# Optimization experiments

Measured on AMD Instinct MI355X. Metric: run time of the kernel, lower is better.

Reference implementation:

```python
import jax, jax.numpy as jnp
import numpy as np

ALPHA = 0.001
RHO = 0.05


def setup_inputs() -> dict:
    key = jax.random.key(0)
    ks = jax.random.split(key, 7)
    S, B, H, L = 1024, 64, 512, 2
    sc = 1.0 / np.sqrt(H)  # torch Linear default init scale
    inputs = jax.random.normal(ks[0], (S, B, H), jnp.float32)
    times = jnp.arange(S, dtype=jnp.float32)
    Wxh_w = jax.random.uniform(ks[1], (L, 4 * H, H), jnp.float32, -sc, sc)
    Wxh_b = jax.random.uniform(ks[2], (L, 4 * H), jnp.float32, -sc, sc)
    Whh_w = jax.random.uniform(ks[3], (L, 4 * H, H), jnp.float32, -sc, sc)
    tau = jax.random.normal(ks[4], (L, H), jnp.float32) * 0.5 + 5.0
    s_p = jax.random.uniform(ks[5], (L, H), jnp.float32) * tau
    return dict(inputs=inputs, times=times, Wxh_w=Wxh_w, Wxh_b=Wxh_b,
                Whh_w=Whh_w, tau=tau, s_p=s_p)


def _time_gate(t, s, tau):
    # phi in [0,1): phase of the oscillation; k is the triangular open-gate
    phi = jnp.fmod(t - s, tau) / tau
    k = jnp.where(phi < RHO / 2.0,
                  2.0 * phi / RHO,
                  jnp.where(phi < RHO, 2.0 - 2.0 * phi / RHO, ALPHA * phi))
    return jax.lax.stop_gradient(k)  # computed under torch.no_grad in source


def reference(inputs, times, Wxh_w, Wxh_b, Whh_w, tau, s_p):
    L, H4, _ = Wxh_w.shape
    H = H4 // 4
    S, B, _ = inputs.shape
    h0 = jnp.zeros((L, B, H), inputs.dtype)
    c0 = jnp.zeros((L, B, H), inputs.dtype)

    def step(carry, xt):
        h, c = carry
        x, t = xt  # x: [B, I], t: scalar time
        new_h, new_c = [], []
        inp = x
        for l in range(L):
            gates = inp @ Wxh_w[l].T + Wxh_b[l] + h[l] @ Whh_w[l].T  # [B, 4H]
            i, f, g, o = jnp.split(gates, 4, axis=1)
            k = _time_gate(t, s_p[l], tau[l])  # [H], broadcasts over batch
            ft = jax.nn.sigmoid(f + 1.0 - k)
            it = jax.nn.sigmoid(i) * k
            gt = jnp.tanh(g) * k
            ot = jax.nn.sigmoid(o) * k
            cy = ft * c[l] + it * gt
            hy = ot * jnp.tanh(cy)
            new_h.append(hy)
            new_c.append(cy)
            inp = hy
        h2 = jnp.stack(new_h)
        c2 = jnp.stack(new_c)
        return (h2, c2), h2[-1]

    (h, c), outputs = jax.lax.scan(step, (h0, c0), (inputs, times))
    return outputs, h, c
```

## Files before the change

kernel.cpp:

```cpp
#include <hip/hip_runtime.h>


#define TPREC 8

#define OFF_H0    4096
#define OFF_H1    266240
#define OFF_H0F   528384
#define OFF_H1F   1052672
#define OFF_C0    1576960
#define OFF_C1    1708032
#define OFF_XPRE  1839104
#define OFF_KTAB  2887680
#define OFF_W0    7081984
#define OFF_W1    9179136
#define OFF_WX    13373440

#define HB_SLOT   65536
#define HF_SLOT   131072
#define XP_SLOT   524288

typedef float  f32x4  __attribute__((ext_vector_type(4)));
typedef int    i32x4  __attribute__((ext_vector_type(4)));
typedef __bf16 bf16x8 __attribute__((ext_vector_type(8)));

static __device__ __forceinline__ unsigned short f2bf(float f) {
  unsigned u = __builtin_bit_cast(unsigned, f);
  u += 0x7FFFu + ((u >> 16) & 1u);
  return (unsigned short)(u >> 16);
}
static __device__ __forceinline__ float sigm(float x) { return 1.0f / (1.0f + __expf(-x)); }
static __device__ __forceinline__ float tanhfast(float x) { return 1.0f - 2.0f / (__expf(2.0f * x) + 1.0f); }

static __device__ __forceinline__ i32x4 ring_load16(const void* p) {
  return *(const i32x4*)p;
}
static __device__ __forceinline__ float ring_loadf(const void* p) {
  return *(const float*)p;
}
static __device__ __forceinline__ void ring_storef(void* p, float v) {
  *(float*)p = v;
}
static __device__ __forceinline__ void ring_store_u16(void* p, unsigned v) {
  *(unsigned short*)p = (unsigned short)v;
}

static __device__ __forceinline__ f32x4 mfma16(bf16x8 a, bf16x8 b, f32x4 c) {
  return __builtin_amdgcn_mfma_f32_16x16x32_bf16(a, b, c, 0, 0, 0);
}
static __device__ __forceinline__ bf16x8 lds_frag(const char* p) {
  return __builtin_bit_cast(bf16x8, *(const i32x4*)p);
}

__global__ void plstm_prep(const float* __restrict__ Wxh_w, const float* __restrict__ Whh_w,
                           const float* __restrict__ times, const float* __restrict__ tau,
                           const float* __restrict__ s_p, unsigned char* __restrict__ ws) {
  const int idx = blockIdx.x * 256 + threadIdx.x;
  const int stride = gridDim.x * 256;
  for (int e = idx; e < 1048576; e += stride) {
    int g = e >> 16, j = (e >> 9) & 127, k = e & 511;
    int gate = j >> 5, u = g * 32 + (j & 31);
    ((unsigned short*)(ws + OFF_W0))[e] = f2bf(Whh_w[(gate * 512 + u) * 512 + k]);
  }
  for (int e = idx; e < 2097152; e += stride) {
    int g = e >> 16, j = (e >> 10) & 63, k = e & 1023;
    int gate = j >> 4, row = gate * 512 + g * 16 + (j & 15);
    float v = (k < 512) ? Wxh_w[1048576 + row * 512 + k] : Whh_w[1048576 + row * 512 + (k - 512)];
    ((unsigned short*)(ws + OFF_W1))[e] = f2bf(v);
  }
  for (int e = idx; e < 1048576; e += stride) {
    int g = e >> 16, j = (e >> 9) & 127, k = e & 511;
    ((unsigned short*)(ws + OFF_WX))[e] = f2bf(Wxh_w[(g * 128 + j) * 512 + k]);
  }
  for (int e = idx; e < 1048576; e += stride) {
    int t = e >> 10, r = e & 1023, l = r >> 9, u = r & 511;
    float phi = fmodf(times[t] - s_p[l * 512 + u], tau[l * 512 + u]) / tau[l * 512 + u];
    float kv;
    if (phi < 0.025f)      kv = phi * 40.0f;
    else if (phi < 0.05f)  kv = 2.0f - phi * 40.0f;
    else                   kv = 0.001f * phi;
    ((float*)(ws + OFF_KTAB))[e] = kv;
  }
}

__global__ void __launch_bounds__(256, 1)
plstm_step(const float* __restrict__ xin, const float* __restrict__ bias,
           const float* __restrict__ Wxh_w, const float* __restrict__ Whh_w,
           float* __restrict__ out, unsigned char* __restrict__ wsu, int q) {
  __shared__ char Wl[131072];
  __shared__ char Al[16384];

  const char* ws = (const char*)wsu;
  char* wsw = (char*)wsu;
  const int bid = blockIdx.x, tid = threadIdx.x;
  const int lane = tid & 63, wv = tid >> 6;
  const int lq = lane >> 4, lr = lane & 15;
  const int role = (bid < 16) ? 0 : (bid < 48) ? 1 : 2;
  const int grp = (role == 0) ? bid : (role == 1) ? bid - 16 : bid - 48;

  if (role == 0 && (q < 1 || q > 1024)) return;
  if (role == 1 && (q < 2 || q > 1025)) return;
  if (role == 2 && q > 1023) return;

  const float* ktabp = (const float*)(ws + OFF_KTAB);
  const float* bias0 = bias;
  const float* bias1 = bias + 2048;
  float* Alf = (float*)Al;

  {
    const char* wsrc = ws +
      ((role == 0) ? (OFF_W0 + grp * 131072) : (role == 1) ? (OFF_W1 + grp * 131072)
                                             : (OFF_WX + grp * 131072));
    const int kshift = (role == 1) ? 10 : 9;
    for (int e = tid * 8; e < 65536; e += 2048) {
      i32x4 v = *(const i32x4*)(wsrc + e * 2);
      int row = e >> kshift;
      *(i32x4*)(Wl + ((e * 2) ^ ((row & 7) << 4))) = v;
    }
    __syncthreads();
  }

  if (role == 0) {
    {
      const int t0 = q - 1;
      const char* xpre = ws + OFF_XPRE + (t0 & 1) * XP_SLOT;
      char* c0p = wsw + OFF_C0;
      char* h0bw = wsw + OFF_H0 + (t0 & 1) * HB_SLOT;

      if (t0 <= TPREC) {
        const int rp = tid >> 4, bq = tid & 15;
        const int gate = rp >> 2;
        const int u0 = grp * 32 + (rp & 3) * 8;
        const float* w8 = Whh_w + (size_t)(gate * 512 + u0) * 512;
        const char* hsrc = ws + OFF_H0F + ((t0 - 1) & 1) * HF_SLOT;
        f32x4 acc8[8] = {};
        for (int kc = 0; kc < 8; ++kc) {
          __syncthreads();
          for (int i = 0; i < 4; ++i) {
            int qi = tid + 256 * i, k = qi >> 4, b4 = qi & 15;
            i32x4 v = ring_load16(hsrc + ((kc * 64 + k) * 64 + b4 * 4) * 4);
            *(i32x4*)(Alf + k * 64 + b4 * 4) = v;
          }
          __syncthreads();
          for (int kb = 0; kb < 16; ++kb) {
            f32x4 w4[8];
#pragma unroll
            for (int r = 0; r < 8; ++r) w4[r] = *(const f32x4*)(w8 + r * 512 + kc * 64 + kb * 4);
#pragma unroll
            for (int ks = 0; ks < 4; ++ks) {
              f32x4 hv = *(const f32x4*)(Alf + (kb * 4 + ks) * 64 + bq * 4);
#pragma unroll
              for (int r = 0; r < 8; ++r) acc8[r] += w4[r][ks] * hv;
            }
          }
        }
        char* h0fw = wsw + OFF_H0F + (t0 & 1) * HF_SLOT;
        for (int ph = 0; ph < 2; ++ph) {
          __syncthreads();
          if ((bq >> 3) == ph) {
#pragma unroll
            for (int r = 0; r < 8; ++r)
              *(f32x4*)(Alf + (rp * 8 + r) * 32 + (bq & 7) * 4) = acc8[r];
          }
          __syncthreads();
          for (int i = 0; i < 4; ++i) {
            int e = tid + 256 * i;
            int u = e >> 5, b32 = e & 31, b = ph * 32 + b32;
            int ucol = grp * 32 + u;
            float g4[4];
#pragma unroll
            for (int gt = 0; gt < 4; ++gt)
              g4[gt] = Alf[(gt * 32 + u) * 32 + b32]
                     + ring_loadf(xpre + (b * 2048 + gt * 512 + ucol) * 4);
            const float kk = ktabp[t0 * 1024 + ucol];
            const float cold = *(const float*)(c0p + (b * 512 + ucol) * 4);
            const float itg = sigm(g4[0]) * kk;
            const float ftg = sigm(g4[1] + 1.0f - kk);
            const float gtg = tanhfast(g4[2]) * kk;
            const float otg = sigm(g4[3]) * kk;
            const float cn = ftg * cold + itg * gtg;
            const float hn = otg * tanhfast(cn);
            *(float*)(c0p + (b * 512 + ucol) * 4) = cn;
            ring_store_u16(h0bw + (b * 512 + ucol) * 2, (unsigned)f2bf(hn));
            ring_storef(h0fw + (ucol * 64 + b) * 4, hn);
          }
        }
      } else {
        const int uf = wv >> 1, mh = wv & 1;
        const int ucol = grp * 32 + uf * 16 + lr;
        float xp[2][4][4];
#pragma unroll
        for (int m = 0; m < 2; ++m)
#pragma unroll
          for (int i = 0; i < 4; ++i) {
            const int b = mh * 32 + m * 16 + lq * 4 + i;
#pragma unroll
            for (int gt = 0; gt < 4; ++gt)
              xp[m][gt][i] = ring_loadf(xpre + (b * 2048 + gt * 512 + ucol) * 4);
          }
        const char* ahi = ws + OFF_H0 + ((t0 - 1) & 1) * HB_SLOT;
        i32x4 areg[16];
#pragma unroll
        for (int kc = 0; kc < 4; ++kc)
#pragma unroll
          for (int it = 0; it < 4; ++it) {
            const int idx = it * 2048 + tid * 8, row = idx >> 7, col = idx & 127;
            areg[kc * 4 + it] = ring_load16(ahi + (row * 512 + kc * 128 + col) * 2);
          }
        const float kk = ktabp[t0 * 1024 + ucol];
        float cold[2][4];
#pragma unroll
        for (int m = 0; m < 2; ++m)
#pragma unroll
          for (int i = 0; i < 4; ++i) {
            const int b = mh * 32 + m * 16 + lq * 4 + i;
            cold[m][i] = *(const float*)(c0p + (b * 512 + ucol) * 4);
          }
        char* c0pw = wsw + OFF_C0;
        f32x4 acc[2][4] = {};
#pragma unroll
        for (int kc = 0; kc < 4; ++kc) {
          __syncthreads();
#pragma unroll
          for (int it = 0; it < 4; ++it) {
            const int idx = it * 2048 + tid * 8, row = idx >> 7, col = idx & 127;
            *(i32x4*)(Al + (((row * 128 + col) * 2) ^ ((row & 7) << 4))) = areg[kc * 4 + it];
          }
          __syncthreads();
#pragma unroll
          for (int ks = 0; ks < 4; ++ks) {
            bf16x8 af[2];
#pragma unroll
            for (int m = 0; m < 2; ++m) {
              const int b = mh * 32 + m * 16 + lr;
              af[m] = lds_frag(Al + (((b * 128 + ks * 32 + lq * 8) * 2) ^ ((b & 7) << 4)));
            }
#pragma unroll
            for (int gt = 0; gt < 4; ++gt) {
              const int j = gt * 32 + uf * 16 + lr;
              const bf16x8 bf = lds_frag(Wl + (((j * 512 + kc * 128 + ks * 32 + lq * 8) * 2) ^ ((j & 7) << 4)));
              acc[0][gt] = mfma16(af[0], bf, acc[0][gt]);
              acc[1][gt] = mfma16(af[1], bf, acc[1][gt]);
            }
          }
        }
#pragma unroll
        for (int m = 0; m < 2; ++m)
#pragma unroll
          for (int i = 0; i < 4; ++i) {
            const int b = mh * 32 + m * 16 + lq * 4 + i;
            const float gi = acc[m][0][i] + xp[m][0][i];
            const float gf = acc[m][1][i] + xp[m][1][i];
            const float gz = acc[m][2][i] + xp[m][2][i];
            const float go = acc[m][3][i] + xp[m][3][i];
            const float itg = sigm(gi) * kk;
            const float ftg = sigm(gf + 1.0f - kk);
            const float gtg = tanhfast(gz) * kk;
            const float otg = sigm(go) * kk;
            const float cn = ftg * cold[m][i] + itg * gtg;
            const float hn = otg * tanhfast(cn);
            *(float*)(c0pw + (b * 512 + ucol) * 4) = cn;
            ring_store_u16(h0bw + (b * 512 + ucol) * 2, (unsigned)f2bf(hn));
            if (t0 == 1023) {
              out[33554432 + b * 512 + ucol] = hn;
              out[33554432 + 65536 + b * 512 + ucol] = cn;
            }
          }
      }
    }
  } else if (role == 1) {
    {
      const int t1 = q - 2;
      char* c1p = wsw + OFF_C1;
      char* h1bw = wsw + OFF_H1 + (t1 & 1) * HB_SLOT;

      if (t1 <= TPREC) {
        const int rp = tid >> 4, bq = tid & 15;
        const int gate = rp >> 2;
        const int uoff0 = (rp & 3) * 4;
        const float* wx4 = Wxh_w + 1048576 + (size_t)(gate * 512 + grp * 16 + uoff0) * 512;
        const float* wh4 = Whh_w + 1048576 + (size_t)(gate * 512 + grp * 16 + uoff0) * 512;
        const char* s0f = ws + OFF_H0F + (t1 & 1) * HF_SLOT;
        const char* s1f = ws + OFF_H1F + ((t1 - 1) & 1) * HF_SLOT;
        f32x4 acc4[4] = {};
        for (int kc = 0; kc < 16; ++kc) {
          const char* hsrc = (kc < 8) ? s0f : s1f;
          const int k0 = (kc & 7) * 64;
          const float* wsel = (kc < 8) ? (wx4 + k0) : (wh4 + k0);
          __syncthreads();
          for (int i = 0; i < 4; ++i) {
            int qi = tid + 256 * i, k = qi >> 4, b4 = qi & 15;
            i32x4 v = ring_load16(hsrc + ((k0 + k) * 64 + b4 * 4) * 4);
            *(i32x4*)(Alf + k * 64 + b4 * 4) = v;
          }
          __syncthreads();
          for (int kb = 0; kb < 16; ++kb) {
            f32x4 w4[4];
#pragma unroll
            for (int r = 0; r < 4; ++r) w4[r] = *(const f32x4*)(wsel + r * 512 + kb * 4);
#pragma unroll
            for (int ks = 0; ks < 4; ++ks) {
              f32x4 hv = *(const f32x4*)(Alf + (kb * 4 + ks) * 64 + bq * 4);
#pragma unroll
              for (int r = 0; r < 4; ++r) acc4[r] += w4[r][ks] * hv;
            }
          }
        }
        char* h1fw = wsw + OFF_H1F + (t1 & 1) * HF_SLOT;
        __syncthreads();
#pragma unroll
        for (int r = 0; r < 4; ++r)
          *(f32x4*)(Alf + (rp * 4 + r) * 64 + bq * 4) = acc4[r];
        __syncthreads();
        for (int i = 0; i < 4; ++i) {
          int e = tid + 256 * i;
          int u = e >> 6, b = e & 63;
          int ucol = grp * 16 + u;
          float g4[4];
#pragma unroll
          for (int gt = 0; gt < 4; ++gt)
            g4[gt] = Alf[(gt * 16 + u) * 64 + b] + bias1[gt * 512 + ucol];
          const float kk = ktabp[t1 * 1024 + 512 + ucol];
          const float cold = *(const float*)(c1p + (b * 512 + ucol) * 4);
          const float itg = sigm(g4[0]) * kk;
          const float ftg = sigm(g4[1] + 1.0f - kk);
          const float gtg = tanhfast(g4[2]) * kk;
          const float otg = sigm(g4[3]) * kk;
          const float cn = ftg * cold + itg * gtg;
          const float hn = otg * tanhfast(cn);
          *(float*)(c1p + (b * 512 + ucol) * 4) = cn;
          ring_store_u16(h1bw + (b * 512 + ucol) * 2, (unsigned)f2bf(hn));
          ring_storef(h1fw + (ucol * 64 + b) * 4, hn);
          out[t1 * 32768 + b * 512 + ucol] = hn;
        }
      } else {
        const int ucol = grp * 16 + lr;
        float bs[4];
#pragma unroll
        for (int gt = 0; gt < 4; ++gt) bs[gt] = bias1[gt * 512 + ucol];
        const float kk = ktabp[t1 * 1024 + 512 + ucol];
        const char* s0 = ws + OFF_H0 + (t1 & 1) * HB_SLOT;
        const char* s1 = ws + OFF_H1 + ((t1 - 1) & 1) * HB_SLOT;
        i32x4 areg[32];
#pragma unroll
        for (int kc = 0; kc < 8; ++kc) {
          const char* s = (kc < 4) ? s0 : s1;
          const int kb = (kc & 3) * 128;
#pragma unroll
          for (int it = 0; it < 4; ++it) {
            const int idx = it * 2048 + tid * 8, row = idx >> 7, col = idx & 127;
            areg[kc * 4 + it] = ring_load16(s + (row * 512 + kb + col) * 2);
          }
        }
        float cold[4];
#pragma unroll
        for (int i = 0; i < 4; ++i) {
          const int b = wv * 16 + lq * 4 + i;
          cold[i] = *(const float*)(c1p + (b * 512 + ucol) * 4);
        }
        f32x4 acc[4] = {};
#pragma unroll
        for (int kc = 0; kc < 8; ++kc) {
          __syncthreads();
#pragma unroll
          for (int it = 0; it < 4; ++it) {
            const int idx = it * 2048 + tid * 8, row = idx >> 7, col = idx & 127;
            *(i32x4*)(Al + (((row * 128 + col) * 2) ^ ((row & 7) << 4))) = areg[kc * 4 + it];
          }
          __syncthreads();
#pragma unroll
          for (int ks = 0; ks < 4; ++ks) {
            const int b = wv * 16 + lr;
            const bf16x8 af = lds_frag(Al + (((b * 128 + ks * 32 + lq * 8) * 2) ^ ((b & 7) << 4)));
#pragma unroll
            for (int gt = 0; gt < 4; ++gt) {
              const int j = gt * 16 + lr;
              const bf16x8 bf = lds_frag(Wl + (((j * 1024 + kc * 128 + ks * 32 + lq * 8) * 2) ^ ((j & 7) << 4)));
              acc[gt] = mfma16(af, bf, acc[gt]);
            }
          }
        }
#pragma unroll
        for (int i = 0; i < 4; ++i) {
          const int b = wv * 16 + lq * 4 + i;
          const float gi = acc[0][i] + bs[0];
          const float gf = acc[1][i] + bs[1];
          const float gz = acc[2][i] + bs[2];
          const float go = acc[3][i] + bs[3];
          const float itg = sigm(gi) * kk;
          const float ftg = sigm(gf + 1.0f - kk);
          const float gtg = tanhfast(gz) * kk;
          const float otg = sigm(go) * kk;
          const float cn = ftg * cold[i] + itg * gtg;
          const float hn = otg * tanhfast(cn);
          *(float*)(c1p + (b * 512 + ucol) * 4) = cn;
          ring_store_u16(h1bw + (b * 512 + ucol) * 2, (unsigned)f2bf(hn));
          out[t1 * 32768 + b * 512 + ucol] = hn;
          if (t1 == 1023) {
            out[33554432 + 32768 + b * 512 + ucol] = hn;
            out[33554432 + 65536 + 32768 + b * 512 + ucol] = cn;
          }
        }
      }
    }
  } else {
    {
      const float* xs = xin + (size_t)q * 32768;
      char* xw = wsw + OFF_XPRE + (q & 1) * XP_SLOT;

      if (q <= TPREC) {
        const int rp = tid >> 4, bq = tid & 15;
        const int n0 = grp * 128 + rp * 8;
        const float* w8 = Wxh_w + (size_t)n0 * 512;
        f32x4 acc8[8] = {};
        for (int kc = 0; kc < 8; ++kc) {
          __syncthreads();
          for (int i = 0; i < 4; ++i) {
            int qi = tid + 256 * i, b = qi >> 4, k4 = qi & 15;
            f32x4 v = *(const f32x4*)(xs + b * 512 + kc * 64 + k4 * 4);
#pragma unroll
            for (int j = 0; j < 4; ++j) Alf[(k4 * 4 + j) * 64 + b] = v[j];
          }
          __syncthreads();
          for (int kb = 0; kb < 16; ++kb) {
            f32x4 w4[8];
#pragma unroll
            for (int r = 0; r < 8; ++r) w4[r] = *(const f32x4*)(w8 + r * 512 + kc * 64 + kb * 4);
#pragma unroll
            for (int ks = 0; ks < 4; ++ks) {
              f32x4 hv = *(const f32x4*)(Alf + (kb * 4 + ks) * 64 + bq * 4);
#pragma unroll
              for (int r = 0; r < 8; ++r) acc8[r] += w4[r][ks] * hv;
            }
          }
        }
#pragma unroll
        for (int r = 0; r < 8; ++r) {
          const int n = n0 + r;
          const float bv = bias0[n];
#pragma unroll
          for (int j = 0; j < 4; ++j)
            ring_storef(xw + ((bq * 4 + j) * 2048 + n) * 4, acc8[r][j] + bv);
        }
      } else {
        float b0v[2];
#pragma unroll
        for (int nf = 0; nf < 2; ++nf) b0v[nf] = bias0[grp * 128 + wv * 32 + nf * 16 + lr];
        f32x4 xr[4][4][2];
#pragma unroll
        for (int kc = 0; kc < 4; ++kc)
#pragma unroll
          for (int it = 0; it < 4; ++it) {
            const int idx = it * 2048 + tid * 8, row = idx >> 7, col = idx & 127;
            const float* p = xs + row * 512 + kc * 128 + col;
            xr[kc][it][0] = *(const f32x4*)p;
            xr[kc][it][1] = *(const f32x4*)(p + 4);
          }
        f32x4 acc[4][2] = {};
#pragma unroll
        for (int kc = 0; kc < 4; ++kc) {
          __syncthreads();
#pragma unroll
          for (int it = 0; it < 4; ++it) {
            const int idx = it * 2048 + tid * 8, row = idx >> 7, col = idx & 127;
            i32x4 v;
#pragma unroll
            for (int w2 = 0; w2 < 4; ++w2) {
              const float x0 = xr[kc][it][w2 >> 1][(w2 & 1) * 2 + 0];
              const float x1 = xr[kc][it][w2 >> 1][(w2 & 1) * 2 + 1];
              v[w2] = (int)((unsigned)f2bf(x0) | ((unsigned)f2bf(x1) << 16));
            }
            *(i32x4*)(Al + (((row * 128 + col) * 2) ^ ((row & 7) << 4))) = v;
          }
          __syncthreads();
#pragma unroll
          for (int ks = 0; ks < 4; ++ks) {
            bf16x8 af[4];
#pragma unroll
            for (int m = 0; m < 4; ++m) {
              const int b = m * 16 + lr;
              af[m] = lds_frag(Al + (((b * 128 + ks * 32 + lq * 8) * 2) ^ ((b & 7) << 4)));
            }
#pragma unroll
            for (int nf = 0; nf < 2; ++nf) {
              const int j = wv * 32 + nf * 16 + lr;
              const bf16x8 bf = lds_frag(Wl + (((j * 512 + kc * 128 + ks * 32 + lq * 8) * 2) ^ ((j & 7) << 4)));
#pragma unroll
              for (int m = 0; m < 4; ++m) acc[m][nf] = mfma16(af[m], bf, acc[m][nf]);
            }
          }
        }
#pragma unroll
        for (int m = 0; m < 4; ++m)
#pragma unroll
          for (int nf = 0; nf < 2; ++nf)
#pragma unroll
            for (int i = 0; i < 4; ++i) {
              const int b = m * 16 + lq * 4 + i;
              const int n = grp * 128 + wv * 32 + nf * 16 + lr;
              ring_storef(xw + (b * 2048 + n) * 4, acc[m][nf][i] + b0v[nf]);
            }
      }
    }
  }
}

extern "C" void kernel_launch(void* const* d_in, const int* in_sizes, int n_in,
                              void* d_out, int out_size, void* d_ws, size_t ws_size,
                              hipStream_t stream) {
  (void)in_sizes; (void)n_in; (void)out_size; (void)ws_size;
  const float* inputs = (const float*)d_in[0];
  const float* times  = (const float*)d_in[1];
  const float* Wxh_w  = (const float*)d_in[2];
  const float* Wxh_b  = (const float*)d_in[3];
  const float* Whh_w  = (const float*)d_in[4];
  const float* tau    = (const float*)d_in[5];
  const float* s_p    = (const float*)d_in[6];
  unsigned char* ws = (unsigned char*)d_ws;
  float* out = (float*)d_out;

  hipMemsetAsync(ws + OFF_H0 + HB_SLOT, 0, HB_SLOT, stream);
  hipMemsetAsync(ws + OFF_H1 + HB_SLOT, 0, HB_SLOT, stream);
  hipMemsetAsync(ws + OFF_H0F + HF_SLOT, 0, HF_SLOT, stream);
  hipMemsetAsync(ws + OFF_H1F + HF_SLOT, 0, HF_SLOT, stream);
  hipMemsetAsync(ws + OFF_C0, 0, 131072, stream);
  hipMemsetAsync(ws + OFF_C1, 0, 131072, stream);

  plstm_prep<<<8192, 256, 0, stream>>>(Wxh_w, Whh_w, times, tau, s_p, ws);

  for (int q = 0; q <= 1025; ++q)
    plstm_step<<<64, 256, 0, stream>>>(inputs, Wxh_b, Wxh_w, Whh_w, out, ws, q);
}
```

Baseline: 12.69 ms.

## Load MFMA operands directly from global memory instead of staging through LDS

Removes the per-launch copy of each block's 128KB weight slice into shared memory and the LDS staging of the hidden/input activation tiles. Each wave now fetches its bf16 A and B fragments straight from global memory (relying on L2/cache), and the input-projection path converts fp32 to bf16 on the fly per fragment. This drops a large LDS fill and several block barriers per step launch, at the cost of redundant, less coalesced global reads across waves.

New measurement: 24.66 ms. 94.3% more time.

```diff
diff --git a/kernel.cpp b/kernel.cpp
--- a/kernel.cpp
+++ b/kernel.cpp
@@ -28,6 +28,9 @@
   u += 0x7FFFu + ((u >> 16) & 1u);
   return (unsigned short)(u >> 16);
 }
+static __device__ __forceinline__ int pack2(float a, float b) {
+  return (int)((unsigned)f2bf(a) | ((unsigned)f2bf(b) << 16));
+}
 static __device__ __forceinline__ float sigm(float x) { return 1.0f / (1.0f + __expf(-x)); }
 static __device__ __forceinline__ float tanhfast(float x) { return 1.0f - 2.0f / (__expf(2.0f * x) + 1.0f); }
 
@@ -47,8 +50,8 @@
 static __device__ __forceinline__ f32x4 mfma16(bf16x8 a, bf16x8 b, f32x4 c) {
   return __builtin_amdgcn_mfma_f32_16x16x32_bf16(a, b, c, 0, 0, 0);
 }
-static __device__ __forceinline__ bf16x8 lds_frag(const char* p) {
-  return __builtin_bit_cast(bf16x8, *(const i32x4*)p);
+static __device__ __forceinline__ bf16x8 asbf(i32x4 v) {
+  return __builtin_bit_cast(bf16x8, v);
 }
 
 __global__ void plstm_prep(const float* __restrict__ Wxh_w, const float* __restrict__ Whh_w,
@@ -86,7 +89,6 @@
 plstm_step(const float* __restrict__ xin, const float* __restrict__ bias,
            const float* __restrict__ Wxh_w, const float* __restrict__ Whh_w,
            float* __restrict__ out, unsigned char* __restrict__ wsu, int q) {
-  __shared__ char Wl[131072];
   __shared__ char Al[16384];
 
   const char* ws = (const char*)wsu;
@@ -105,19 +107,6 @@
   const float* bias0 = bias;
   const float* bias1 = bias + 2048;
   float* Alf = (float*)Al;
-
-  {
-    const char* wsrc = ws +
-      ((role == 0) ? (OFF_W0 + grp * 131072) : (role == 1) ? (OFF_W1 + grp * 131072)
-                                             : (OFF_WX + grp * 131072));
-    const int kshift = (role == 1) ? 10 : 9;
-    for (int e = tid * 8; e < 65536; e += 2048) {
-      i32x4 v = *(const i32x4*)(wsrc + e * 2);
-      int row = e >> kshift;
-      *(i32x4*)(Wl + ((e * 2) ^ ((row & 7) << 4))) = v;
-    }
-    __syncthreads();
-  }
 
   if (role == 0) {
     {
@@ -187,6 +176,7 @@
       } else {
         const int uf = wv >> 1, mh = wv & 1;
         const int ucol = grp * 32 + uf * 16 + lr;
+        const char* w0src = ws + OFF_W0 + grp * 131072;
         float xp[2][4][4];
 #pragma unroll
         for (int m = 0; m < 2; ++m)
@@ -198,14 +188,6 @@
               xp[m][gt][i] = ring_loadf(xpre + (b * 2048 + gt * 512 + ucol) * 4);
           }
         const char* ahi = ws + OFF_H0 + ((t0 - 1) & 1) * HB_SLOT;
-        i32x4 areg[16];
-#pragma unroll
-        for (int kc = 0; kc < 4; ++kc)
-#pragma unroll
-          for (int it = 0; it < 4; ++it) {
-            const int idx = it * 2048 + tid * 8, row = idx >> 7, col = idx & 127;
-            areg[kc * 4 + it] = ring_load16(ahi + (row * 512 + kc * 128 + col) * 2);
-          }
         const float kk = ktabp[t0 * 1024 + ucol];
         float cold[2][4];
 #pragma unroll
@@ -215,29 +197,22 @@
             const int b = mh * 32 + m * 16 + lq * 4 + i;
             cold[m][i] = *(const float*)(c0p + (b * 512 + ucol) * 4);
           }
-        char* c0pw = wsw + OFF_C0;
         f32x4 acc[2][4] = {};
 #pragma unroll
         for (int kc = 0; kc < 4; ++kc) {
-          __syncthreads();
-#pragma unroll
-          for (int it = 0; it < 4; ++it) {
-            const int idx = it * 2048 + tid * 8, row = idx >> 7, col = idx & 127;
-            *(i32x4*)(Al + (((row * 128 + col) * 2) ^ ((row & 7) << 4))) = areg[kc * 4 + it];
-          }
-          __syncthreads();
 #pragma unroll
           for (int ks = 0; ks < 4; ++ks) {
+            const int ko = kc * 128 + ks * 32 + lq * 8;
             bf16x8 af[2];
 #pragma unroll
             for (int m = 0; m < 2; ++m) {
               const int b = mh * 32 + m * 16 + lr;
-              af[m] = lds_frag(Al + (((b * 128 + ks * 32 + lq * 8) * 2) ^ ((b & 7) << 4)));
+              af[m] = asbf(ring_load16(ahi + (b * 512 + ko) * 2));
             }
 #pragma unroll
             for (int gt = 0; gt < 4; ++gt) {
               const int j = gt * 32 + uf * 16 + lr;
-              const bf16x8 bf = lds_frag(Wl + (((j * 512 + kc * 128 + ks * 32 + lq * 8) * 2) ^ ((j & 7) << 4)));
+              const bf16x8 bf = asbf(ring_load16(w0src + (j * 512 + ko) * 2));
               acc[0][gt] = mfma16(af[0], bf, acc[0][gt]);
               acc[1][gt] = mfma16(af[1], bf, acc[1][gt]);
             }
@@ -258,7 +233,7 @@
             const float otg = sigm(go) * kk;
             const float cn = ftg * cold[m][i] + itg * gtg;
             const float hn = otg * tanhfast(cn);
-            *(float*)(c0pw + (b * 512 + ucol) * 4) = cn;
+            *(float*)(c0p + (b * 512 + ucol) * 4) = cn;
             ring_store_u16(h0bw + (b * 512 + ucol) * 2, (unsigned)f2bf(hn));
             if (t0 == 1023) {
               out[33554432 + b * 512 + ucol] = hn;
@@ -334,47 +309,33 @@
         }
       } else {
         const int ucol = grp * 16 + lr;
+        const char* w1src = ws + OFF_W1 + grp * 131072;
         float bs[4];
 #pragma unroll
         for (int gt = 0; gt < 4; ++gt) bs[gt] = bias1[gt * 512 + ucol];
         const float kk = ktabp[t1 * 1024 + 512 + ucol];
         const char* s0 = ws + OFF_H0 + (t1 & 1) * HB_SLOT;
         const char* s1 = ws + OFF_H1 + ((t1 - 1) & 1) * HB_SLOT;
-        i32x4 areg[32];
+        const int brow = wv * 16 + lr;
+        float cold[4];
+#pragma unroll
+        for (int i = 0; i < 4; ++i) {
+          const int b = wv * 16 + lq * 4 + i;
+          cold[i] = *(const float*)(c1p + (b * 512 + ucol) * 4);
+        }
+        f32x4 acc[4] = {};
 #pragma unroll
         for (int kc = 0; kc < 8; ++kc) {
           const char* s = (kc < 4) ? s0 : s1;
           const int kb = (kc & 3) * 128;
 #pragma unroll
-          for (int it = 0; it < 4; ++it) {
-            const int idx = it * 2048 + tid * 8, row = idx >> 7, col = idx & 127;
-            areg[kc * 4 + it] = ring_load16(s + (row * 512 + kb + col) * 2);
-          }
-        }
-        float cold[4];
-#pragma unroll
-        for (int i = 0; i < 4; ++i) {
-          const int b = wv * 16 + lq * 4 + i;
-          cold[i] = *(const float*)(c1p + (b * 512 + ucol) * 4);
-        }
-        f32x4 acc[4] = {};
-#pragma unroll
-        for (int kc = 0; kc < 8; ++kc) {
-          __syncthreads();
-#pragma unroll
-          for (int it = 0; it < 4; ++it) {
-            const int idx = it * 2048 + tid * 8, row = idx >> 7, col = idx & 127;
-            *(i32x4*)(Al + (((row * 128 + col) * 2) ^ ((row & 7) << 4))) = areg[kc * 4 + it];
-          }
-          __syncthreads();
-#pragma unroll
           for (int ks = 0; ks < 4; ++ks) {
-            const int b = wv * 16 + lr;
-            const bf16x8 af = lds_frag(Al + (((b * 128 + ks * 32 + lq * 8) * 2) ^ ((b & 7) << 4)));
+            const int ko = kb + ks * 32 + lq * 8;
+            const bf16x8 af = asbf(ring_load16(s + (brow * 512 + ko) * 2));
 #pragma unroll
             for (int gt = 0; gt < 4; ++gt) {
               const int j = gt * 16 + lr;
-              const bf16x8 bf = lds_frag(Wl + (((j * 1024 + kc * 128 + ks * 32 + lq * 8) * 2) ^ ((j & 7) << 4)));
+              const bf16x8 bf = asbf(ring_load16(w1src + (j * 1024 + kc * 128 + ks * 32 + lq * 8) * 2));
               acc[gt] = mfma16(af, bf, acc[gt]);
             }
           }
@@ -442,48 +403,31 @@
             ring_storef(xw + ((bq * 4 + j) * 2048 + n) * 4, acc8[r][j] + bv);
         }
       } else {
+        const char* wxsrc = ws + OFF_WX + grp * 131072;
         float b0v[2];
 #pragma unroll
         for (int nf = 0; nf < 2; ++nf) b0v[nf] = bias0[grp * 128 + wv * 32 + nf * 16 + lr];
-        f32x4 xr[4][4][2];
-#pragma unroll
-        for (int kc = 0; kc < 4; ++kc)
-#pragma unroll
-          for (int it = 0; it < 4; ++it) {
-            const int idx = it * 2048 + tid * 8, row = idx >> 7, col = idx & 127;
-            const float* p = xs + row * 512 + kc * 128 + col;
-            xr[kc][it][0] = *(const f32x4*)p;
-            xr[kc][it][1] = *(const f32x4*)(p + 4);
-          }
         f32x4 acc[4][2] = {};
 #pragma unroll
         for (int kc = 0; kc < 4; ++kc) {
-          __syncthreads();
-#pragma unroll
-          for (int it = 0; it < 4; ++it) {
-            const int idx = it * 2048 + tid * 8, row = idx >> 7, col = idx & 127;
-            i32x4 v;
-#pragma unroll
-            for (int w2 = 0; w2 < 4; ++w2) {
-              const float x0 = xr[kc][it][w2 >> 1][(w2 & 1) * 2 + 0];
-              const float x1 = xr[kc][it][w2 >> 1][(w2 & 1) * 2 + 1];
-              v[w2] = (int)((unsigned)f2bf(x0) | ((unsigned)f2bf(x1) << 16));
-            }
-            *(i32x4*)(Al + (((row * 128 + col) * 2) ^ ((row & 7) << 4))) = v;
-          }
-          __syncthreads();
 #pragma unroll
           for (int ks = 0; ks < 4; ++ks) {
+            const int ko = kc * 128 + ks * 32 + lq * 8;
             bf16x8 af[4];
 #pragma unroll
             for (int m = 0; m < 4; ++m) {
-              const int b = m * 16 + lr;
-              af[m] = lds_frag(Al + (((b * 128 + ks * 32 + lq * 8) * 2) ^ ((b & 7) << 4)));
+              const float* p = xs + (m * 16 + lr) * 512 + ko;
+              const f32x4 lo = *(const f32x4*)p;
+              const f32x4 hi = *(const f32x4*)(p + 4);
+              i32x4 v;
+              v[0] = pack2(lo[0], lo[1]); v[1] = pack2(lo[2], lo[3]);
+              v[2] = pack2(hi[0], hi[1]); v[3] = pack2(hi[2], hi[3]);
+              af[m] = asbf(v);
             }
 #pragma unroll
             for (int nf = 0; nf < 2; ++nf) {
               const int j = wv * 32 + nf * 16 + lr;
-              const bf16x8 bf = lds_frag(Wl + (((j * 512 + kc * 128 + ks * 32 + lq * 8) * 2) ^ ((j & 7) << 4)));
+              const bf16x8 bf = asbf(ring_load16(wxsrc + (j * 512 + ko) * 2));
 #pragma unroll
               for (int m = 0; m < 4; ++m) acc[m][nf] = mfma16(af[m], bf, acc[m][nf]);
             }
```
